# Kernel tuning notes

Hardware: AMD Instinct MI355X
Metric: run time of the kernel (lower is better)

Reference implementation:

```python
import jax, jax.numpy as jnp
import numpy as np

NUM_HEADS = 16
EMBED_DIM = 1024
HEAD_DIM = EMBED_DIM // NUM_HEADS
SCALE = HEAD_DIM * -0.5  # faithful to source: multiplicative, negative


def setup_inputs() -> dict:
    key = jax.random.key(0)
    kx, kq, kk, kv, ko = jax.random.split(key, 5)
    B, S, E = 2, 2048, EMBED_DIM
    std = 1.0 / np.sqrt(E)
    return {
        "x": jax.random.normal(kx, (B, S, E), dtype=jnp.float32),
        "Wq": jax.random.normal(kq, (E, E), dtype=jnp.float32) * std,
        "Wk": jax.random.normal(kk, (E, E), dtype=jnp.float32) * std,
        "Wv": jax.random.normal(kv, (E, E), dtype=jnp.float32) * std,
        "Wo": jax.random.normal(ko, (E, E), dtype=jnp.float32) * std,
    }


def reference(x, Wq, Wk, Wv, Wo):
    B, S, E = x.shape
    H, D = NUM_HEADS, HEAD_DIM
    # nn.Linear(bias=False): y = x @ W.T
    q = (x @ Wq.T).reshape(B, S, H, D).transpose(0, 2, 1, 3)  # unused downstream (faithful to source)
    k = (x @ Wk.T).reshape(B, S, H, D).transpose(0, 2, 1, 3)  # [B,H,S,D]
    v = (x @ Wv.T).reshape(B, S, H, D).transpose(0, 2, 1, 3)
    # Source bug reproduced: logits = K @ V^T, scaled by head_dim * -0.5
    logits = jnp.einsum('bhsd,bhtd->bhst', k, v) * SCALE  # [B,H,S,S]
    attn = jax.nn.softmax(logits, axis=-1)
    out = jnp.einsum('bhst,bhtd->bhsd', attn, v)  # [B,H,S,D]
    out = out.transpose(0, 2, 1, 3).reshape(B, S, E)
    return out @ Wo.T
```

## Files before the change

kernel.cpp:

```cpp
#include <hip/hip_runtime.h>
#include <math.h>

#define B_ 2
#define S_ 2048
#define E_ 1024
#define H_ 16
#define D_ 64
#define M_ (B_ * S_)
#define SC2 (-46.166241308446828f)

typedef unsigned short u16;
typedef _Float16 f16;
typedef __attribute__((ext_vector_type(8))) _Float16 f16x8;
typedef __attribute__((ext_vector_type(2))) __fp16 fp16x2_n;
typedef __attribute__((ext_vector_type(16))) float f32x16;

static __device__ __forceinline__ f32x16 mfma_h(f16x8 a, f16x8 b, f32x16 c) {
    return __builtin_amdgcn_mfma_f32_32x32x16_f16(a, b, c, 0, 0, 0);
}
static __device__ __forceinline__ u16 f16bits(f16 h) {
    union { f16 h; u16 u; } c; c.h = h; return c.u;
}
static __device__ __forceinline__ unsigned pack2(u16 a, u16 b) {
    return (unsigned)a | ((unsigned)b << 16);
}
static __device__ __forceinline__ unsigned pkrtz(float a, float b) {
    fp16x2_n h = __builtin_amdgcn_cvt_pkrtz(a, b);
    unsigned u; __builtin_memcpy(&u, &h, 4); return u;
}
static __device__ __forceinline__ void pl32swap(unsigned &a, unsigned &b) {
    asm volatile("v_permlane32_swap_b32 %0, %1" : "+v"(a), "+v"(b));
}
#define ROWMAP(r, hh) (((r) & 3) + ((((r) >> 2)) << 3) + ((hh) << 2))

__global__ __launch_bounds__(256)
void convert_split(const float* __restrict__ x, const float* __restrict__ Wk,
                   const float* __restrict__ Wv, const float* __restrict__ Wo,
                   u16* __restrict__ Xh, u16* __restrict__ Xl,
                   u16* __restrict__ Wkh, u16* __restrict__ Wkl,
                   u16* __restrict__ Wvh, u16* __restrict__ Wvl,
                   u16* __restrict__ Woh)
{
    const int blk = blockIdx.x;
    const float* src; u16 *dh, *dl; int base; float sc = 1.0f; bool wantlo = true;
    if (blk < 4096)      { src = x;  dh = Xh;  dl = Xl;  base = blk; }
    else if (blk < 5120) { src = Wk; dh = Wkh; dl = Wkl; base = blk - 4096; sc = SC2; }
    else if (blk < 6144) { src = Wv; dh = Wvh; dl = Wvl; base = blk - 5120; }
    else                 { src = Wo; dh = Woh; dl = Woh; base = blk - 6144; wantlo = false; }
    const size_t off = ((size_t)base * 256 + threadIdx.x) * 4;
    const float4 v = *(const float4*)(src + off);
    const float f[4] = {v.x * sc, v.y * sc, v.z * sc, v.w * sc};
    u16 h4[4], l4[4];
#pragma unroll
    for (int i = 0; i < 4; ++i) {
        const f16 h = (f16)f[i];
        h4[i] = f16bits(h);
        l4[i] = f16bits((f16)(f[i] - (float)h));
    }
    *(uint2*)(dh + off) = make_uint2(pack2(h4[0], h4[1]), pack2(h4[2], h4[3]));
    if (wantlo)
        *(uint2*)(dl + off) = make_uint2(pack2(l4[0], l4[1]), pack2(l4[2], l4[3]));
}

#define CSB 1032

template<int MODE>
__global__ __launch_bounds__(1024, 4)
void gemm_f(const u16* __restrict__ Ah_, const u16* __restrict__ Al_,
            const u16* __restrict__ Bkh_, const u16* __restrict__ Bkl_,
            const u16* __restrict__ Bvh_, const u16* __restrict__ Bvl_,
            u16* __restrict__ Khg, u16* __restrict__ Klg,
            u16* __restrict__ Vhg, u16* __restrict__ Vtg,
            float* __restrict__ Cout)
{
    constexpr int BK   = (MODE == 0 ? 64 : 128);
    constexpr int NCH  = BK / 8;
    constexpr int NKK  = NCH / 4;
    constexpr int ARRX = NCH * CSB;
    constexpr int NIT  = E_ / BK;
    extern __shared__ u16 stage[];

    const int tid = threadIdx.x;
    const int w = tid >> 6, l31 = tid & 31, hh = (tid >> 5) & 1;
    const int wt = w & 7, ws = w >> 3;
    const int wm = (wt >> 1) << 5, wn = (wt & 1) << 6;
    const int m0 = blockIdx.y * 128, n0 = blockIdx.x * 128;
    const int ch8 = (ws << 1) + hh;

    const int sr = tid >> 3, sch = tid & 7;
    const size_t gA = (size_t)(m0 + sr) * E_ + (sch << 3);
    const size_t gB = (size_t)(n0 + sr) * E_ + (sch << 3);
    const int slo = sch * CSB + sr * 8;

    f32x16 acc1[2], acc2[2];
#pragma unroll
    for (int nt = 0; nt < 2; ++nt)
#pragma unroll
        for (int r = 0; r < 16; ++r) {
            acc1[nt][r] = 0.f;
            if constexpr (MODE == 0) acc2[nt][r] = 0.f;
        }

    constexpr int NPF = (MODE == 0 ? 6 : 4);
    f16x8 pf[NPF];
    auto load_tile = [&](int k0) {
        if constexpr (MODE == 0) {
            pf[0] = *(const f16x8*)(Ah_ + gA + k0);
            pf[1] = *(const f16x8*)(Al_ + gA + k0);
            pf[2] = *(const f16x8*)(Bkh_ + gB + k0);
            pf[3] = *(const f16x8*)(Bkl_ + gB + k0);
            pf[4] = *(const f16x8*)(Bvh_ + gB + k0);
            pf[5] = *(const f16x8*)(Bvl_ + gB + k0);
        } else {
            pf[0] = *(const f16x8*)(Ah_ + gA + k0);
            pf[1] = *(const f16x8*)(Ah_ + gA + k0 + 64);
            pf[2] = *(const f16x8*)(Bkh_ + gB + k0);
            pf[3] = *(const f16x8*)(Bkh_ + gB + k0 + 64);
        }
    };
    auto store_tile = [&](int bb) {
        if constexpr (MODE == 0) {
#pragma unroll
            for (int a = 0; a < 6; ++a)
                *(f16x8*)&stage[bb + a * ARRX + slo] = pf[a];
        } else {
            *(f16x8*)&stage[bb + slo] = pf[0];
            *(f16x8*)&stage[bb + (sch + 8) * CSB + sr * 8] = pf[1];
            *(f16x8*)&stage[bb + ARRX + slo] = pf[2];
            *(f16x8*)&stage[bb + ARRX + (sch + 8) * CSB + sr * 8] = pf[3];
        }
    };
    auto compute = [&](int bb) {
#pragma unroll
        for (int kk = 0; kk < NKK; ++kk) {
            const int co = bb + (ch8 + (kk << 2)) * CSB;
            const int offx = co + (wm + l31) * 8;
            const f16x8 xh = *(const f16x8*)&stage[0 * ARRX + offx];
            f16x8 xl;
            if constexpr (MODE == 0) xl = *(const f16x8*)&stage[1 * ARRX + offx];
#pragma unroll
            for (int nt = 0; nt < 2; ++nt) {
                const int ro = co + (wn + (nt << 5) + l31) * 8;
                if constexpr (MODE == 0) {
                    const f16x8 bkh = *(const f16x8*)&stage[2 * ARRX + ro];
                    const f16x8 bkl = *(const f16x8*)&stage[3 * ARRX + ro];
                    const f16x8 bvh = *(const f16x8*)&stage[4 * ARRX + ro];
                    const f16x8 bvl = *(const f16x8*)&stage[5 * ARRX + ro];
                    acc1[nt] = mfma_h(xh, bkh, acc1[nt]);
                    acc1[nt] = mfma_h(xh, bkl, acc1[nt]);
                    acc1[nt] = mfma_h(xl, bkh, acc1[nt]);
                    acc2[nt] = mfma_h(xh, bvh, acc2[nt]);
                    acc2[nt] = mfma_h(xh, bvl, acc2[nt]);
                    acc2[nt] = mfma_h(xl, bvh, acc2[nt]);
                } else {
                    const f16x8 bh = *(const f16x8*)&stage[ARRX + ro];
                    acc1[nt] = mfma_h(xh, bh, acc1[nt]);
                }
            }
        }
    };

    if constexpr (MODE == 0) {
        load_tile(0);
        for (int it = 0; it < NIT; ++it) {
            store_tile(0);
            __syncthreads();
            if (it + 1 < NIT) load_tile((it + 1) * BK);
            compute(0);
            __syncthreads();
        }
    } else {
        load_tile(0);
        store_tile(0);
        __syncthreads();
        for (int it = 0; it < NIT; ++it) {
            const int cb = (it & 1) * (2 * ARRX);
            const int nb = ((it + 1) & 1) * (2 * ARRX);
            if (it + 1 < NIT) load_tile((it + 1) * BK);
            compute(cb);
            if (it + 1 < NIT) store_tile(nb);
            __syncthreads();
        }
    }

    float* red = (float*)stage;
    constexpr int NR = (MODE == 0 ? 4 : 2);
#pragma unroll
    for (int rd = 0; rd < NR; ++rd) {
        const int ntr = rd & 1;
        f32x16* A = (MODE == 0 && rd >= 2) ? &acc2[ntr] : &acc1[ntr];
        __syncthreads();
        if (ws == 1) {
#pragma unroll
            for (int r = 0; r < 16; ++r)
                red[(wt << 10) + (r << 6) + (hh << 5) + l31] = (*A)[r];
        }
        __syncthreads();
        if (ws == 0) {
#pragma unroll
            for (int r = 0; r < 16; ++r)
                (*A)[r] += red[(wt << 10) + (r << 6) + (hh << 5) + l31];
        }
    }
    if (ws != 0) return;

#pragma unroll
    for (int nt = 0; nt < 2; ++nt) {
        const int n = n0 + wn + (nt << 5) + l31;
        if constexpr (MODE == 1) {
#pragma unroll
            for (int r = 0; r < 16; ++r) {
                const int m = m0 + wm + ROWMAP(r, hh);
                Cout[(size_t)m * E_ + n] = acc1[nt][r];
            }
        } else {
            const int hd = n >> 6, d = n & 63;
            const int b = m0 >> 11;
            u16 vb16[16];
#pragma unroll
            for (int r = 0; r < 16; ++r) {
                const int s = (m0 + wm + ROWMAP(r, hh)) & (S_ - 1);
                const size_t ib = (((size_t)(b * H_ + hd) << 11) + s) * D_ + d;
                const float kv = acc1[nt][r];
                const f16 kh = (f16)kv;
                Khg[ib] = f16bits(kh);
                Klg[ib] = f16bits((f16)(kv - (float)kh));
                const f16 vh = (f16)acc2[nt][r];
                vb16[r] = f16bits(vh);
                Vhg[ib] = vb16[r];
            }
            const size_t vtb = ((size_t)(b * H_ + hd) * D_ + d) << 11;
#pragma unroll
            for (int g = 0; g < 4; ++g) {
                const int s0 = ((m0 + wm) & (S_ - 1)) + (g << 3) + (hh << 2);
                *(uint2*)&Vtg[vtb + s0] =
                    make_uint2(pack2(vb16[4 * g], vb16[4 * g + 1]),
                               pack2(vb16[4 * g + 2], vb16[4 * g + 3]));
            }
        }
    }
}

#define CSA 520
#define VA  (8 * CSA)

__global__ __launch_bounds__(512, 2)
void attn_mfma(const u16* __restrict__ Kh, const u16* __restrict__ Kl,
               const u16* __restrict__ Vh, const u16* __restrict__ Vt,
               u16* __restrict__ Obuf)
{
    __shared__ u16 sV[4 * VA];

    const int tid = threadIdx.x;
    const int w = tid >> 6, l31 = tid & 31, hh = (tid >> 5) & 1;
    const int bh = blockIdx.y;
    const int sbase = blockIdx.x * 256 + (w << 5);
    const int sg = sbase + l31;

    f16x8 kfh[4], kfl[4];
    {
        const size_t kb = ((size_t)bh * S_ + sg) * D_;
#pragma unroll
        for (int ks = 0; ks < 4; ++ks) {
            const int db = (ks << 4) + (hh << 3);
            kfh[ks] = *(const f16x8*)(Kh + kb + db);
            kfl[ks] = *(const f16x8*)(Kl + kb + db);
        }
    }

    f32x16 oacc[2];
#pragma unroll
    for (int r = 0; r < 16; ++r) { oacc[0][r] = 0.f; oacc[1][r] = 0.f; }
    float m_i = -INFINITY, l_i = 0.f;

    const int rr = tid >> 3, cc = tid & 7;
    const size_t gn = ((size_t)bh * S_ + rr) * D_ + (cc << 3);
    const size_t gt = ((size_t)bh * D_ + rr) * S_ + (cc << 3);
    const int slo = cc * CSA + rr * 8;

    f16x8 pv[2];
    auto load_tile = [&](int it2) {
        const size_t t0 = (size_t)it2 << 6;
        pv[0] = *(const f16x8*)(Vh + gn + t0 * D_);
        pv[1] = *(const f16x8*)(Vt + gt + t0);
    };

    load_tile(0);
    *(f16x8*)&sV[slo] = pv[0];
    *(f16x8*)&sV[VA + slo] = pv[1];
    __syncthreads();

    for (int it = 0; it < 32; ++it) {
        const int vb = (it & 1) * (2 * VA);
        const int nb = ((it + 1) & 1) * (2 * VA);
        if (it + 1 < 32) load_tile(it + 1);

        f32x16 sta[2], stb[2];
#pragma unroll
        for (int r = 0; r < 16; ++r) {
            sta[0][r] = 0.f; sta[1][r] = 0.f;
            stb[0][r] = 0.f; stb[1][r] = 0.f;
        }
#pragma unroll
        for (int ks = 0; ks < 4; ++ks) {
            const int ch = (ks << 1) + hh;
#pragma unroll
            for (int mt = 0; mt < 2; ++mt) {
                const f16x8 av = *(const f16x8*)&sV[vb + ch * CSA + ((mt << 5) + l31) * 8];
                sta[mt] = mfma_h(av, kfh[ks], sta[mt]);
                stb[mt] = mfma_h(av, kfl[ks], stb[mt]);
            }
        }
#pragma unroll
        for (int mt = 0; mt < 2; ++mt)
#pragma unroll
            for (int r = 0; r < 16; ++r) sta[mt][r] += stb[mt][r];

        float tmax = -INFINITY;
#pragma unroll
        for (int mt = 0; mt < 2; ++mt)
#pragma unroll
            for (int r = 0; r < 16; ++r) tmax = fmaxf(tmax, sta[mt][r]);
        tmax = fmaxf(tmax, __shfl_xor(tmax, 32));
        const float mnew = fmaxf(m_i, tmax);
        const float alpha = __builtin_amdgcn_exp2f(m_i - mnew);
        m_i = mnew;
        const unsigned long long cmask = __ballot(tmax >= mnew - 30.f);

        if (cmask) {
            float rsum = 0.f;
#pragma unroll
            for (int mt = 0; mt < 2; ++mt)
#pragma unroll
                for (int r = 0; r < 16; ++r) {
                    const float p = __builtin_amdgcn_exp2f(sta[mt][r] - mnew);
                    sta[mt][r] = p;
                    rsum += p;
                }
            rsum += __shfl_xor(rsum, 32);
            l_i = l_i * alpha + rsum;

#pragma unroll
            for (int r = 0; r < 16; ++r) { oacc[0][r] *= alpha; oacc[1][r] *= alpha; }

            unsigned pa[2][4], pb[2][4];
#pragma unroll
            for (int mt = 0; mt < 2; ++mt)
#pragma unroll
                for (int q = 0; q < 4; ++q) {
                    pa[mt][q] = pkrtz(sta[mt][4 * q + 0], sta[mt][4 * q + 1]);
                    pb[mt][q] = pkrtz(sta[mt][4 * q + 2], sta[mt][4 * q + 3]);
                }

#pragma unroll
            for (int ks = 0; ks < 4; ++ks) {
                const int mt = ks >> 1, kk = ks & 1;
                unsigned w0 = pa[mt][2 * kk], w2v = pa[mt][2 * kk + 1];
                pl32swap(w0, w2v);
                unsigned w1 = pb[mt][2 * kk], w3v = pb[mt][2 * kk + 1];
                pl32swap(w1, w3v);
                union { unsigned u[4]; f16x8 v; } bw;
                bw.u[0] = w0; bw.u[1] = w1; bw.u[2] = w2v; bw.u[3] = w3v;
                const int ch = (ks << 1) + hh;
#pragma unroll
                for (int nt = 0; nt < 2; ++nt) {
                    const f16x8 vtf = *(const f16x8*)&sV[vb + VA + ch * CSA + ((nt << 5) + l31) * 8];
                    oacc[nt] = mfma_h(vtf, bw.v, oacc[nt]);
                }
            }
        }

        if (it + 1 < 32) {
            *(f16x8*)&sV[nb + slo] = pv[0];
            *(f16x8*)&sV[nb + VA + slo] = pv[1];
        }
        __syncthreads();
    }

    const float linv = (l_i > 0.f) ? (1.0f / l_i) : 0.f;
    const int b = bh >> 4;
    const int hd = bh & 15;
    u16* Or = Obuf + ((size_t)b * S_ + sg) * E_ + (hd << 6);
#pragma unroll
    for (int nt = 0; nt < 2; ++nt)
#pragma unroll
        for (int q = 0; q < 4; ++q) {
            const int d0 = (nt << 5) + (q << 3) + (hh << 2);
            u16 c[4];
#pragma unroll
            for (int j = 0; j < 4; ++j)
                c[j] = f16bits((f16)(oacc[nt][4 * q + j] * linv));
            *(uint2*)&Or[d0] = make_uint2(pack2(c[0], c[1]), pack2(c[2], c[3]));
        }
}

extern "C" void kernel_launch(void* const* d_in, const int* in_sizes, int n_in,
                              void* d_out, int out_size, void* d_ws, size_t ws_size,
                              hipStream_t stream)
{
    (void)in_sizes; (void)n_in; (void)out_size; (void)ws_size;
    const float* x  = (const float*)d_in[0];
    const float* Wk = (const float*)d_in[2];
    const float* Wv = (const float*)d_in[3];
    const float* Wo = (const float*)d_in[4];
    float* out = (float*)d_out;

    char* ws = (char*)d_ws;
    const size_t MB = 1u << 20;
    u16* Xh  = (u16*)(ws + 0 * MB);
    u16* Xl  = (u16*)(ws + 8 * MB);
    u16* Wkh = (u16*)(ws + 16 * MB);
    u16* Wkl = (u16*)(ws + 18 * MB);
    u16* Wvh = (u16*)(ws + 20 * MB);
    u16* Wvl = (u16*)(ws + 22 * MB);
    u16* Woh = (u16*)(ws + 24 * MB);
    u16* Kh  = (u16*)(ws + 26 * MB);
    u16* Kl  = (u16*)(ws + 34 * MB);
    u16* Vh  = (u16*)(ws + 42 * MB);
    u16* Vt  = (u16*)(ws + 50 * MB);
    u16* Obuf = Xl;

    const int lds0 = 6 * (8 * CSB) * (int)sizeof(u16);
    const int lds1 = 2 * 2 * (16 * CSB) * (int)sizeof(u16);
    static bool attr_done = false;
    if (!attr_done) {
        hipFuncSetAttribute(reinterpret_cast<const void*>(&gemm_f<0>),
                            hipFuncAttributeMaxDynamicSharedMemorySize, lds0);
        hipFuncSetAttribute(reinterpret_cast<const void*>(&gemm_f<1>),
                            hipFuncAttributeMaxDynamicSharedMemorySize, lds1);
        attr_done = true;
    }

    convert_split<<<7168, 256, 0, stream>>>(x, Wk, Wv, Wo,
                                            Xh, Xl, Wkh, Wkl, Wvh, Wvl, Woh);
    gemm_f<0><<<dim3(E_ / 128, M_ / 128), 1024, lds0, stream>>>(
        Xh, Xl, Wkh, Wkl, Wvh, Wvl, Kh, Kl, Vh, Vt, nullptr);
    attn_mfma<<<dim3(S_ / 256, B_ * H_), 512, 0, stream>>>(Kh, Kl, Vh, Vt, Obuf);
    gemm_f<1><<<dim3(E_ / 128, M_ / 128), 1024, lds1, stream>>>(
        Obuf, Obuf, Woh, Woh, Woh, Woh,
        nullptr, nullptr, nullptr, nullptr, out);
}
```

Measured before the change: 216.8 us.

## Deepen global prefetch to two register tiles and use LDS-only barriers

Replaces __syncthreads with a barrier that waits only on LDS/scalar counters (lgkmcnt), so outstanding global loads no longer have to drain at each barrier. The GEMM (mode 1) and attention loops are unrolled by two with ping-pong register prefetch buffers, keeping two tiles of global loads in flight while computing. This is meant to hide global memory latency behind MFMA work, at the cost of more VGPRs, which may lower occupancy. It also assumes NIT is even.

After: 209.4 us. 1.04x faster.

```diff
diff --git a/kernel.cpp b/kernel.cpp
--- a/kernel.cpp
+++ b/kernel.cpp
@@ -30,6 +30,10 @@
 }
 static __device__ __forceinline__ void pl32swap(unsigned &a, unsigned &b) {
     asm volatile("v_permlane32_swap_b32 %0, %1" : "+v"(a), "+v"(b));
+}
+static __device__ __forceinline__ void lgkm_bar() {
+    asm volatile("s_waitcnt lgkmcnt(0)" ::: "memory");
+    __builtin_amdgcn_s_barrier();
 }
 #define ROWMAP(r, hh) (((r) & 3) + ((((r) >> 2)) << 3) + ((hh) << 2))
 
@@ -102,8 +106,8 @@
         }
 
     constexpr int NPF = (MODE == 0 ? 6 : 4);
-    f16x8 pf[NPF];
-    auto load_tile = [&](int k0) {
+    f16x8 pf0[NPF], pf1[NPF];
+    auto load_tile = [&](int k0, f16x8* pf) {
         if constexpr (MODE == 0) {
             pf[0] = *(const f16x8*)(Ah_ + gA + k0);
             pf[1] = *(const f16x8*)(Al_ + gA + k0);
@@ -118,7 +122,7 @@
             pf[3] = *(const f16x8*)(Bkh_ + gB + k0 + 64);
         }
     };
-    auto store_tile = [&](int bb) {
+    auto store_tile = [&](int bb, f16x8* pf) {
         if constexpr (MODE == 0) {
 #pragma unroll
             for (int a = 0; a < 6; ++a)
@@ -161,25 +165,29 @@
     };
 
     if constexpr (MODE == 0) {
-        load_tile(0);
+        load_tile(0, pf0);
         for (int it = 0; it < NIT; ++it) {
-            store_tile(0);
-            __syncthreads();
-            if (it + 1 < NIT) load_tile((it + 1) * BK);
+            store_tile(0, pf0);
+            lgkm_bar();
+            if (it + 1 < NIT) load_tile((it + 1) * BK, pf0);
             compute(0);
-            __syncthreads();
+            lgkm_bar();
         }
     } else {
-        load_tile(0);
-        store_tile(0);
-        __syncthreads();
-        for (int it = 0; it < NIT; ++it) {
-            const int cb = (it & 1) * (2 * ARRX);
-            const int nb = ((it + 1) & 1) * (2 * ARRX);
-            if (it + 1 < NIT) load_tile((it + 1) * BK);
-            compute(cb);
-            if (it + 1 < NIT) store_tile(nb);
-            __syncthreads();
+        load_tile(0, pf0);
+        store_tile(0, pf0);
+        load_tile(BK, pf1);
+        lgkm_bar();
+        for (int p = 0; p < NIT / 2; ++p) {
+            const int e = 2 * p;
+            if (e + 2 < NIT) load_tile((e + 2) * BK, pf0);
+            compute(0);
+            store_tile(2 * ARRX, pf1);
+            lgkm_bar();
+            if (e + 3 < NIT) load_tile((e + 3) * BK, pf1);
+            compute(2 * ARRX);
+            if (e + 2 < NIT) store_tile(0, pf0);
+            lgkm_bar();
         }
     }
 
@@ -278,23 +286,18 @@
     const size_t gt = ((size_t)bh * D_ + rr) * S_ + (cc << 3);
     const int slo = cc * CSA + rr * 8;
 
-    f16x8 pv[2];
-    auto load_tile = [&](int it2) {
+    f16x8 pv0[2], pv1[2];
+    auto load_t = [&](int it2, f16x8* pv) {
         const size_t t0 = (size_t)it2 << 6;
         pv[0] = *(const f16x8*)(Vh + gn + t0 * D_);
         pv[1] = *(const f16x8*)(Vt + gt + t0);
     };
-
-    load_tile(0);
-    *(f16x8*)&sV[slo] = pv[0];
-    *(f16x8*)&sV[VA + slo] = pv[1];
-    __syncthreads();
-
-    for (int it = 0; it < 32; ++it) {
-        const int vb = (it & 1) * (2 * VA);
-        const int nb = ((it + 1) & 1) * (2 * VA);
-        if (it + 1 < 32) load_tile(it + 1);
-
+    auto store_t = [&](int nb, f16x8* pv) {
+        *(f16x8*)&sV[nb + slo] = pv[0];
+        *(f16x8*)&sV[nb + VA + slo] = pv[1];
+    };
+
+    auto PROC = [&](int base) {
         f32x16 sta[2], stb[2];
 #pragma unroll
         for (int r = 0; r < 16; ++r) {
@@ -306,7 +309,7 @@
             const int ch = (ks << 1) + hh;
 #pragma unroll
             for (int mt = 0; mt < 2; ++mt) {
-                const f16x8 av = *(const f16x8*)&sV[vb + ch * CSA + ((mt << 5) + l31) * 8];
+                const f16x8 av = *(const f16x8*)&sV[base + ch * CSA + ((mt << 5) + l31) * 8];
                 sta[mt] = mfma_h(av, kfh[ks], sta[mt]);
                 stb[mt] = mfma_h(av, kfl[ks], stb[mt]);
             }
@@ -364,17 +367,28 @@
                 const int ch = (ks << 1) + hh;
 #pragma unroll
                 for (int nt = 0; nt < 2; ++nt) {
-                    const f16x8 vtf = *(const f16x8*)&sV[vb + VA + ch * CSA + ((nt << 5) + l31) * 8];
+                    const f16x8 vtf = *(const f16x8*)&sV[base + VA + ch * CSA + ((nt << 5) + l31) * 8];
                     oacc[nt] = mfma_h(vtf, bw.v, oacc[nt]);
                 }
             }
         }
-
-        if (it + 1 < 32) {
-            *(f16x8*)&sV[nb + slo] = pv[0];
-            *(f16x8*)&sV[nb + VA + slo] = pv[1];
-        }
-        __syncthreads();
+    };
+
+    load_t(0, pv0);
+    store_t(0, pv0);
+    load_t(1, pv1);
+    lgkm_bar();
+
+    for (int p = 0; p < 16; ++p) {
+        const int e = 2 * p;
+        if (e + 2 < 32) load_t(e + 2, pv0);
+        PROC(0);
+        store_t(2 * VA, pv1);
+        lgkm_bar();
+        if (e + 3 < 32) load_t(e + 3, pv1);
+        PROC(2 * VA);
+        if (e + 2 < 32) store_t(0, pv0);
+        lgkm_bar();
     }
 
     const float linv = (l_i > 0.f) ? (1.0f / l_i) : 0.f;
```
